# Performance work log

Measured on AMD Instinct MI355X. Metric: run time of the kernel, lower is better.

The kernel has to match this reference:

```python
import math
import jax, jax.numpy as jnp
import numpy as np

N, E = 20000, 640000
S_DIM, Z_DIM, H, QK, VD = 64, 64, 4, 8, 8
EPS = 1e-8


def quat_rotate(v, q):
    # v: [..., 3], q: [..., 4] (w, x, y, z), broadcastable. Unit-quaternion rotation:
    # v' = v + 2*(w*(u x v) + u x (u x v))
    w = q[..., 0:1]
    u = q[..., 1:4]
    uv = jnp.cross(u, v)
    return v + 2.0 * (w * uv + jnp.cross(u, uv))


def setup_inputs() -> dict:
    key = jax.random.key(0)
    ks = jax.random.split(key, 16)
    s = jax.random.normal(ks[0], (N, S_DIM), dtype=jnp.float32)
    z = jax.random.normal(ks[1], (E, Z_DIM), dtype=jnp.float32)
    edge_index = jax.random.randint(ks[2], (2, E), 0, N)
    quaternion = jax.random.normal(ks[3], (N, 4), dtype=jnp.float32)
    quaternion = quaternion / jnp.linalg.norm(quaternion, axis=-1, keepdims=True)
    translation = jax.random.normal(ks[4], (N, 3), dtype=jnp.float32)
    sc_s = 1.0 / math.sqrt(S_DIM)
    sc_z = 1.0 / math.sqrt(Z_DIM)
    # weights stored [in, out] so y = x @ W (equivalent to torch x @ W.T)
    Wq_s = jax.random.normal(ks[5], (S_DIM, H * S_DIM), dtype=jnp.float32) * sc_s
    Wk_s = jax.random.normal(ks[6], (S_DIM, H * S_DIM), dtype=jnp.float32) * sc_s
    Wv_s = jax.random.normal(ks[7], (S_DIM, H * S_DIM), dtype=jnp.float32) * sc_s
    Wq_v = jax.random.normal(ks[8], (S_DIM, H * QK * 3), dtype=jnp.float32) * sc_s
    Wk_v = jax.random.normal(ks[9], (S_DIM, H * QK * 3), dtype=jnp.float32) * sc_s
    Wv_v = jax.random.normal(ks[10], (S_DIM, H * VD * 3), dtype=jnp.float32) * sc_s
    Wb = jax.random.normal(ks[11], (Z_DIM, H), dtype=jnp.float32) * sc_z
    bb = jnp.zeros((H,), dtype=jnp.float32)
    Wdz = jax.random.normal(ks[12], (Z_DIM, Z_DIM // 4), dtype=jnp.float32) * sc_z
    bdz = jnp.zeros((Z_DIM // 4,), dtype=jnp.float32)
    head_weights = jnp.full((H,), 0.541324854612918, dtype=jnp.float32)  # softplus^{-1}(1)
    concat_dim = Z_DIM // 4 + S_DIM + VD * 4
    Wout = jax.random.normal(ks[13], (H * concat_dim, S_DIM), dtype=jnp.float32) / math.sqrt(H * concat_dim)
    bout = jnp.zeros((S_DIM,), dtype=jnp.float32)
    return {
        's': s, 'z': z, 'edge_index': edge_index, 'quaternion': quaternion,
        'translation': translation, 'Wq_s': Wq_s, 'Wk_s': Wk_s, 'Wv_s': Wv_s,
        'Wq_v': Wq_v, 'Wk_v': Wk_v, 'Wv_v': Wv_v, 'Wb': Wb, 'bb': bb,
        'Wdz': Wdz, 'bdz': bdz, 'head_weights': head_weights,
        'Wout': Wout, 'bout': bout,
    }


def reference(s, z, edge_index, quaternion, translation,
              Wq_s, Wk_s, Wv_s, Wq_v, Wk_v, Wv_v,
              Wb, bb, Wdz, bdz, head_weights, Wout, bout):
    idx_i, idx_j = edge_index[0], edge_index[1]
    n = s.shape[0]
    h = head_weights.shape[0]
    qk = Wq_v.shape[1] // (3 * h)
    vd = Wv_v.shape[1] // (3 * h)

    q_scalar = (s @ Wq_s).reshape(n, h, -1)
    k_scalar = (s @ Wk_s).reshape(n, h, -1)
    v_scalar = (s @ Wv_s).reshape(n, h, -1)

    def to_points(x):
        # torch.split into 3 chunks then stack(dim=-1): [n, 3*c] -> [n, c, 3]
        c = x.shape[-1] // 3
        return jnp.swapaxes(x.reshape(n, 3, c), 1, 2)

    quat_b = quaternion[:, None, :]
    trans_b = translation[:, None, :]
    q_vec = (quat_rotate(to_points(s @ Wq_v), quat_b) + trans_b).reshape(n, h, qk, 3)
    k_vec = (quat_rotate(to_points(s @ Wk_v), quat_b) + trans_b).reshape(n, h, qk, 3)
    v_vec = (quat_rotate(to_points(s @ Wv_v), quat_b) + trans_b).reshape(n, h, vd, 3)

    b_bias = z @ Wb + bb  # [E, H]

    attn = jnp.sum(k_scalar[idx_i] * q_scalar[idx_j], axis=-1)  # [E, H]
    attn = attn * math.sqrt(1.0 / 3 * qk) + math.sqrt(1.0 / 3) * b_bias

    disp = q_vec[idx_i] - k_vec[idx_j]            # [E, H, qk, 3]
    vec_att = jnp.sum(disp * disp, axis=-1)       # [E, H, qk]
    hw = jax.nn.softplus(head_weights)[None, :, None]
    vec_att = jnp.sum(vec_att * hw, axis=-1) * math.sqrt(1.0 / (3 * (qk * 9.0 / 2))) * (-0.5)
    attn = attn + vec_att

    # segment softmax over destination node idx_i
    seg_max = jax.ops.segment_max(attn, idx_i, num_segments=n)
    ea = jnp.exp(attn - seg_max[idx_i])
    denom = jax.ops.segment_sum(ea, idx_i, num_segments=n)
    attn = ea / denom[idx_i]                      # [E, H]

    out_scalar = jax.ops.segment_sum(attn[:, :, None] * v_scalar[idx_i], idx_i, num_segments=n)
    out_scalar = out_scalar.reshape(n, -1)

    out_vec = jax.ops.segment_sum(attn[:, :, None, None] * v_vec[idx_i], idx_i, num_segments=n)
    out_vec = out_vec - translation[:, None, None, :]
    q_conj = jnp.concatenate([quaternion[:, :1], -quaternion[:, 1:]], axis=-1)
    out_vec = quat_rotate(out_vec, q_conj[:, None, None, :])   # [n, h, vd, 3]
    out_vec_norm = jnp.sqrt(jnp.sum(out_vec * out_vec, axis=-1) + EPS).reshape(n, -1)
    out_vec_flat = out_vec.reshape(n, -1, 3)

    pair_z = z @ Wdz + bdz                         # [E, z/4]
    out_pair = jax.ops.segment_sum(attn[:, :, None] * pair_z[:, None, :], idx_i, num_segments=n)
    out_pair = out_pair.reshape(n, -1)

    feats = jnp.concatenate([out_scalar,
                             out_vec_flat[..., 0], out_vec_flat[..., 1], out_vec_flat[..., 2],
                             out_vec_norm, out_pair], axis=-1)
    return feats @ Wout + bout
```

## Files before the change

### kernel.cpp

```cpp
#include <hip/hip_runtime.h>
#include <stdint.h>


#define C_SQRT83  1.6329931618554518f
#define C_SQRT13  0.5773502691896258f
#define C_VEC    -0.04811252243246881f

__device__ __forceinline__ unsigned short f2bf(float f){
  unsigned u = __float_as_uint(f);
  u += 0x7fffu + ((u >> 16) & 1u);
  return (unsigned short)(u >> 16);
}
__device__ __forceinline__ unsigned pack2(float a, float b){
  return (unsigned)f2bf(a) | ((unsigned)f2bf(b) << 16);
}
__device__ __forceinline__ float bflo(unsigned u){ return __uint_as_float(u << 16); }
__device__ __forceinline__ float bfhi(unsigned u){ return __uint_as_float(u & 0xffff0000u); }

__device__ __forceinline__ void quat_rot(float w, float ux, float uy, float uz,
                                         float vx, float vy, float vz,
                                         float& ox, float& oy, float& oz){
  float cx = uy*vz - uz*vy;
  float cy = uz*vx - ux*vz;
  float cz = ux*vy - uy*vx;
  float dx = uy*cz - uz*cy;
  float dy = uz*cx - ux*cz;
  float dz = ux*cy - uy*cx;
  ox = vx + 2.f*(w*cx + dx);
  oy = vy + 2.f*(w*cy + dy);
  oz = vz + 2.f*(w*cz + dz);
}


__global__ __launch_bounds__(256) void k_count(const int* __restrict__ ei,
                                               unsigned* __restrict__ counts,
                                               unsigned* __restrict__ rank, int ne){
  int e = blockIdx.x*256 + threadIdx.x;
  if (e >= ne) return;
  rank[e] = atomicAdd(&counts[ei[e]], 1u);
}

__global__ __launch_bounds__(256) void k_scan(const unsigned* __restrict__ counts,
                                              unsigned* __restrict__ row_off, int n){
  __shared__ unsigned part[256];
  int t = threadIdx.x;
  int chunk = (n + 255) >> 8;
  int s0 = t*chunk, s1 = min(s0 + chunk, n);
  unsigned sum = 0;
  for (int k = s0; k < s1; ++k) sum += counts[k];
  part[t] = sum; __syncthreads();
  for (int off = 1; off < 256; off <<= 1){
    unsigned v = (t >= off) ? part[t-off] : 0u;
    __syncthreads();
    part[t] += v;
    __syncthreads();
  }
  unsigned run = (t == 0) ? 0u : part[t-1];
  for (int k = s0; k < s1; ++k){
    row_off[k] = run; run += counts[k];
  }
  if (t == 255) row_off[n] = part[255];
}


#define BN 32

__device__ __forceinline__ void pass256(const float* __restrict__ W,
                                        const float stT[64][40], int cg, int sl,
                                        float acc[8][4]){
  #pragma unroll
  for (int i=0;i<8;i++){ acc[i][0]=0.f; acc[i][1]=0.f; acc[i][2]=0.f; acc[i][3]=0.f; }
  #pragma unroll 4
  for (int k = 0; k < 64; ++k){
    const float4 w  = *(const float4*)(W + (size_t)k*256 + cg*4);
    const float4 n0 = *(const float4*)&stT[k][sl*8];
    const float4 n1 = *(const float4*)&stT[k][sl*8+4];
    acc[0][0]+=n0.x*w.x; acc[0][1]+=n0.x*w.y; acc[0][2]+=n0.x*w.z; acc[0][3]+=n0.x*w.w;
    acc[1][0]+=n0.y*w.x; acc[1][1]+=n0.y*w.y; acc[1][2]+=n0.y*w.z; acc[1][3]+=n0.y*w.w;
    acc[2][0]+=n0.z*w.x; acc[2][1]+=n0.z*w.y; acc[2][2]+=n0.z*w.z; acc[2][3]+=n0.z*w.w;
    acc[3][0]+=n0.w*w.x; acc[3][1]+=n0.w*w.y; acc[3][2]+=n0.w*w.z; acc[3][3]+=n0.w*w.w;
    acc[4][0]+=n1.x*w.x; acc[4][1]+=n1.x*w.y; acc[4][2]+=n1.x*w.z; acc[4][3]+=n1.x*w.w;
    acc[5][0]+=n1.y*w.x; acc[5][1]+=n1.y*w.y; acc[5][2]+=n1.y*w.z; acc[5][3]+=n1.y*w.w;
    acc[6][0]+=n1.z*w.x; acc[6][1]+=n1.z*w.y; acc[6][2]+=n1.z*w.z; acc[6][3]+=n1.z*w.w;
    acc[7][0]+=n1.w*w.x; acc[7][1]+=n1.w*w.y; acc[7][2]+=n1.w*w.z; acc[7][3]+=n1.w*w.w;
  }
}

__device__ __forceinline__ void pass96(const float* __restrict__ W,
                                       const float stT[64][40], int cgp, int slp,
                                       float acc[4][4]){
  #pragma unroll
  for (int i=0;i<4;i++){ acc[i][0]=0.f; acc[i][1]=0.f; acc[i][2]=0.f; acc[i][3]=0.f; }
  if (cgp >= 24) return;
  #pragma unroll 4
  for (int k = 0; k < 64; ++k){
    const float4 w = *(const float4*)(W + (size_t)k*96 + cgp*4);
    const float4 nv = *(const float4*)&stT[k][slp*4];
    acc[0][0]+=nv.x*w.x; acc[0][1]+=nv.x*w.y; acc[0][2]+=nv.x*w.z; acc[0][3]+=nv.x*w.w;
    acc[1][0]+=nv.y*w.x; acc[1][1]+=nv.y*w.y; acc[1][2]+=nv.y*w.z; acc[1][3]+=nv.y*w.w;
    acc[2][0]+=nv.z*w.x; acc[2][1]+=nv.z*w.y; acc[2][2]+=nv.z*w.z; acc[2][3]+=nv.z*w.w;
    acc[3][0]+=nv.w*w.x; acc[3][1]+=nv.w*w.y; acc[3][2]+=nv.w*w.z; acc[3][3]+=nv.w*w.w;
  }
}

__global__ __launch_bounds__(256) void k_proj(
    const float* __restrict__ s, const float* __restrict__ quat, const float* __restrict__ trans,
    const float* __restrict__ Wqs, const float* __restrict__ Wks, const float* __restrict__ Wvs,
    const float* __restrict__ Wqv, const float* __restrict__ Wkv, const float* __restrict__ Wvv,
    unsigned* __restrict__ qs, unsigned* __restrict__ ks, float* __restrict__ vs,
    unsigned* __restrict__ qv, unsigned* __restrict__ kv, float* __restrict__ vv, int n)
{
  __shared__ float stT[64][40];
  __shared__ float pt[BN][97];
  const int tid = threadIdx.x;
  const int node0 = blockIdx.x * BN;

  #pragma unroll
  for (int r = 0; r < 2; ++r){
    const int idx = tid + r*256;
    const int nd = idx >> 4, c4 = idx & 15;
    const int g = node0 + nd;
    float4 v = make_float4(0.f,0.f,0.f,0.f);
    if (g < n) v = *(const float4*)(s + (size_t)g*64 + c4*4);
    stT[c4*4+0][nd]=v.x; stT[c4*4+1][nd]=v.y; stT[c4*4+2][nd]=v.z; stT[c4*4+3][nd]=v.w;
  }
  __syncthreads();

  const int cg = tid & 63, sl = tid >> 6;
  const int cgp = tid & 31, slp = tid >> 5;
  float acc[8][4];

  pass256(Wqs, stT, cg, sl, acc);
  #pragma unroll
  for (int i=0;i<8;i++){
    const int g = node0 + sl*8 + i;
    if (g < n){
      uint2 u; u.x = pack2(acc[i][0],acc[i][1]); u.y = pack2(acc[i][2],acc[i][3]);
      *(uint2*)(qs + (size_t)g*128 + cg*2) = u;
    }
  }
  pass256(Wks, stT, cg, sl, acc);
  #pragma unroll
  for (int i=0;i<8;i++){
    const int g = node0 + sl*8 + i;
    if (g < n){
      uint2 u; u.x = pack2(acc[i][0],acc[i][1]); u.y = pack2(acc[i][2],acc[i][3]);
      *(uint2*)(ks + (size_t)g*128 + cg*2) = u;
    }
  }
  pass256(Wvs, stT, cg, sl, acc);
  #pragma unroll
  for (int i=0;i<8;i++){
    const int g = node0 + sl*8 + i;
    if (g < n){
      float4 f; f.x=acc[i][0]; f.y=acc[i][1]; f.z=acc[i][2]; f.w=acc[i][3];
      *(float4*)(vs + (size_t)g*256 + cg*4) = f;
    }
  }

  float pac[4][4];

  pass96(Wqv, stT, cgp, slp, pac);
  __syncthreads();
  if (cgp < 24){
    #pragma unroll
    for (int i=0;i<4;i++){
      #pragma unroll
      for (int c=0;c<4;c++) pt[slp*4+i][cgp*4+c] = pac[i][c];
    }
  }
  __syncthreads();
  #pragma unroll
  for (int r = 0; r < 2; ++r){
    const int t2 = tid + r*256;
    const int nd = t2 >> 4, pp = t2 & 15;
    const int g = node0 + nd;
    if (g < n){
      const float4 q4 = *(const float4*)(quat + (size_t)g*4);
      const float tx = trans[(size_t)g*3], ty = trans[(size_t)g*3+1], tz = trans[(size_t)g*3+2];
      float x0,y0,z0,x1,y1,z1;
      quat_rot(q4.x,q4.y,q4.z,q4.w, pt[nd][2*pp],   pt[nd][32+2*pp],   pt[nd][64+2*pp],   x0,y0,z0);
      quat_rot(q4.x,q4.y,q4.z,q4.w, pt[nd][2*pp+1], pt[nd][32+2*pp+1], pt[nd][64+2*pp+1], x1,y1,z1);
      x0+=tx; y0+=ty; z0+=tz; x1+=tx; y1+=ty; z1+=tz;
      unsigned* d = qv + (size_t)g*48 + pp*3;
      d[0] = pack2(x0,y0); d[1] = pack2(z0,x1); d[2] = pack2(y1,z1);
    }
  }

  pass96(Wkv, stT, cgp, slp, pac);
  __syncthreads();
  if (cgp < 24){
    #pragma unroll
    for (int i=0;i<4;i++){
      #pragma unroll
      for (int c=0;c<4;c++) pt[slp*4+i][cgp*4+c] = pac[i][c];
    }
  }
  __syncthreads();
  #pragma unroll
  for (int r = 0; r < 2; ++r){
    const int t2 = tid + r*256;
    const int nd = t2 >> 4, pp = t2 & 15;
    const int g = node0 + nd;
    if (g < n){
      const float4 q4 = *(const float4*)(quat + (size_t)g*4);
      const float tx = trans[(size_t)g*3], ty = trans[(size_t)g*3+1], tz = trans[(size_t)g*3+2];
      float x0,y0,z0,x1,y1,z1;
      quat_rot(q4.x,q4.y,q4.z,q4.w, pt[nd][2*pp],   pt[nd][32+2*pp],   pt[nd][64+2*pp],   x0,y0,z0);
      quat_rot(q4.x,q4.y,q4.z,q4.w, pt[nd][2*pp+1], pt[nd][32+2*pp+1], pt[nd][64+2*pp+1], x1,y1,z1);
      x0+=tx; y0+=ty; z0+=tz; x1+=tx; y1+=ty; z1+=tz;
      unsigned* d = kv + (size_t)g*48 + pp*3;
      d[0] = pack2(x0,y0); d[1] = pack2(z0,x1); d[2] = pack2(y1,z1);
    }
  }

  pass96(Wvv, stT, cgp, slp, pac);
  __syncthreads();
  if (cgp < 24){
    #pragma unroll
    for (int i=0;i<4;i++){
      #pragma unroll
      for (int c=0;c<4;c++) pt[slp*4+i][cgp*4+c] = pac[i][c];
    }
  }
  __syncthreads();
  #pragma unroll
  for (int r = 0; r < 12; ++r){
    const int idx = tid + r*256;
    const int nd = idx / 96, col = idx - nd*96;
    const int g = node0 + nd;
    if (g < n) vv[(size_t)g*96 + col] = pt[nd][col];
  }
}


__global__ __launch_bounds__(256) void k_zc(
    const int* __restrict__ ei, const unsigned* __restrict__ rank,
    const unsigned* __restrict__ roff, const float* __restrict__ z,
    const float* __restrict__ Wb,  const float* __restrict__ bb,
    const float* __restrict__ Wdz, const float* __restrict__ bdz,
    const float* __restrict__ hwts,
    const unsigned* __restrict__ qs, const unsigned* __restrict__ ks,
    const unsigned* __restrict__ qv, const unsigned* __restrict__ kv,
    unsigned* __restrict__ rec, int ne)
{
  __shared__ float zT[2][16][258];
  const int tid = threadIdx.x;
  const int E0  = blockIdx.x * 256;
  const int e   = E0 + tid;
  const bool full = (E0 + 256 <= ne);

  int i = 0, j = 0; unsigned pos = 0;
  if (e < ne){
    i = ei[e]; j = ei[ne + e];
    pos = roff[i] + rank[e];
  }

  const float hw0 = C_VEC * log1pf(__expf(hwts[0]));
  const float hw1 = C_VEC * log1pf(__expf(hwts[1]));
  const float hw2 = C_VEC * log1pf(__expf(hwts[2]));
  const float hw3 = C_VEC * log1pf(__expf(hwts[3]));

  float b4[4] = {0.f,0.f,0.f,0.f};
  float pacc[16];
  #pragma unroll
  for (int c=0;c<16;c++) pacc[c]=0.f;

  if (full){
    #pragma unroll
    for (int q = 0; q < 4; ++q){
      const int idx = tid + q*256;
      const int row = idx >> 2, f4 = idx & 3;
      const float4 v = *(const float4*)(z + (size_t)(E0+row)*64 + f4*4);
      zT[0][f4*4+0][row]=v.x; zT[0][f4*4+1][row]=v.y;
      zT[0][f4*4+2][row]=v.z; zT[0][f4*4+3][row]=v.w;
    }
    __syncthreads();
    #pragma unroll
    for (int c = 0; c < 4; ++c){
      if (c < 3){
        const int nb = (c+1)&1;
        #pragma unroll
        for (int q = 0; q < 4; ++q){
          const int idx = tid + q*256;
          const int row = idx >> 2, f4 = idx & 3;
          const float4 v = *(const float4*)(z + (size_t)(E0+row)*64 + (c+1)*16 + f4*4);
          zT[nb][f4*4+0][row]=v.x; zT[nb][f4*4+1][row]=v.y;
          zT[nb][f4*4+2][row]=v.z; zT[nb][f4*4+3][row]=v.w;
        }
      }
      const int kb = c*16, buf = c&1;
      #pragma unroll
      for (int kk = 0; kk < 16; ++kk){
        const float zk = zT[buf][kk][tid];
        const int k = kb + kk;
        const float4 wb = *(const float4*)(Wb + k*4);
        b4[0]+=zk*wb.x; b4[1]+=zk*wb.y; b4[2]+=zk*wb.z; b4[3]+=zk*wb.w;
        const float* wd = Wdz + k*16;
        const float4 w0=*(const float4*)(wd),   w1=*(const float4*)(wd+4),
                     w2=*(const float4*)(wd+8), w3=*(const float4*)(wd+12);
        pacc[ 0]+=zk*w0.x; pacc[ 1]+=zk*w0.y; pacc[ 2]+=zk*w0.z; pacc[ 3]+=zk*w0.w;
        pacc[ 4]+=zk*w1.x; pacc[ 5]+=zk*w1.y; pacc[ 6]+=zk*w1.z; pacc[ 7]+=zk*w1.w;
        pacc[ 8]+=zk*w2.x; pacc[ 9]+=zk*w2.y; pacc[10]+=zk*w2.z; pacc[11]+=zk*w2.w;
        pacc[12]+=zk*w3.x; pacc[13]+=zk*w3.y; pacc[14]+=zk*w3.z; pacc[15]+=zk*w3.w;
      }
      __syncthreads();
    }
  } else if (e < ne){
    const float* zr = z + (size_t)e*64;
    for (int k4 = 0; k4 < 16; ++k4){
      const float4 zv = *(const float4*)(zr + 4*k4);
      #pragma unroll
      for (int kk = 0; kk < 4; ++kk){
        const int k = 4*k4 + kk;
        const float zk = (kk==0)?zv.x:((kk==1)?zv.y:((kk==2)?zv.z:zv.w));
        const float4 wb = *(const float4*)(Wb + k*4);
        b4[0]+=zk*wb.x; b4[1]+=zk*wb.y; b4[2]+=zk*wb.z; b4[3]+=zk*wb.w;
        const float* wd = Wdz + k*16;
        const float4 w0=*(const float4*)(wd),   w1=*(const float4*)(wd+4),
                     w2=*(const float4*)(wd+8), w3=*(const float4*)(wd+12);
        pacc[ 0]+=zk*w0.x; pacc[ 1]+=zk*w0.y; pacc[ 2]+=zk*w0.z; pacc[ 3]+=zk*w0.w;
        pacc[ 4]+=zk*w1.x; pacc[ 5]+=zk*w1.y; pacc[ 6]+=zk*w1.z; pacc[ 7]+=zk*w1.w;
        pacc[ 8]+=zk*w2.x; pacc[ 9]+=zk*w2.y; pacc[10]+=zk*w2.z; pacc[11]+=zk*w2.w;
        pacc[12]+=zk*w3.x; pacc[13]+=zk*w3.y; pacc[14]+=zk*w3.z; pacc[15]+=zk*w3.w;
      }
    }
  }

  uint4 u0, u1;
  float bl0=0.f, bl1=0.f, bl2=0.f, bl3=0.f;
  if (e < ne){
    #pragma unroll
    for (int c=0;c<16;c++) pacc[c] += bdz[c];
    u0.x=pack2(pacc[0],pacc[1]);   u0.y=pack2(pacc[2],pacc[3]);
    u0.z=pack2(pacc[4],pacc[5]);   u0.w=pack2(pacc[6],pacc[7]);
    u1.x=pack2(pacc[8],pacc[9]);   u1.y=pack2(pacc[10],pacc[11]);
    u1.z=pack2(pacc[12],pacc[13]); u1.w=pack2(pacc[14],pacc[15]);
    bl0 = C_SQRT13*(b4[0] + bb[0]);
    bl1 = C_SQRT13*(b4[1] + bb[1]);
    bl2 = C_SQRT13*(b4[2] + bb[2]);
    bl3 = C_SQRT13*(b4[3] + bb[3]);
  } else {
    u0 = make_uint4(0,0,0,0); u1 = make_uint4(0,0,0,0);
  }

  if (full){
    const int l = tid & 63;
    const int c = l & 3, g = l >> 2;
    #pragma unroll
    for (int sb = 0; sb < 4; ++sb){
      const int el = sb*16 + g;
      const int ie = __shfl(i, el, 64);
      const int je = __shfl(j, el, 64);

      const uint4* kr = (const uint4*)ks + (size_t)ie*32;
      const uint4* qr = (const uint4*)qs + (size_t)je*32;
      float s0=0.f, s1=0.f, s2=0.f, s3=0.f;
      #pragma unroll
      for (int it = 0; it < 8; ++it){
        const uint4 a = kr[it*4 + c];
        const uint4 b = qr[it*4 + c];
        float d;
        d  = bflo(a.x)*bflo(b.x) + bfhi(a.x)*bfhi(b.x);
        d += bflo(a.y)*bflo(b.y) + bfhi(a.y)*bfhi(b.y);
        d += bflo(a.z)*bflo(b.z) + bfhi(a.z)*bfhi(b.z);
        d += bflo(a.w)*bflo(b.w) + bfhi(a.w)*bfhi(b.w);
        if      (it < 2) s0 += d;
        else if (it < 4) s1 += d;
        else if (it < 6) s2 += d;
        else             s3 += d;
      }

      const uint4* qvr = (const uint4*)qv + (size_t)ie*12;
      const uint4* kvr = (const uint4*)kv + (size_t)je*12;
      float v0=0.f, v1=0.f, v2=0.f, v3=0.f;
      {
        const uint4 a = qvr[c], b = kvr[c];
        float d, t;
        t = bflo(a.x)-bflo(b.x); d  = t*t;  t = bfhi(a.x)-bfhi(b.x); d += t*t;
        t = bflo(a.y)-bflo(b.y); d += t*t;  t = bfhi(a.y)-bfhi(b.y); d += t*t;
        t = bflo(a.z)-bflo(b.z); d += t*t;  t = bfhi(a.z)-bfhi(b.z); d += t*t;
        t = bflo(a.w)-bflo(b.w); d += t*t;  t = bfhi(a.w)-bfhi(b.w); d += t*t;
        if (c < 3) v0 += d; else v1 += d;
      }
      {
        const uint4 a = qvr[4+c], b = kvr[4+c];
        float d, t;
        t = bflo(a.x)-bflo(b.x); d  = t*t;  t = bfhi(a.x)-bfhi(b.x); d += t*t;
        t = bflo(a.y)-bflo(b.y); d += t*t;  t = bfhi(a.y)-bfhi(b.y); d += t*t;
        t = bflo(a.z)-bflo(b.z); d += t*t;  t = bfhi(a.z)-bfhi(b.z); d += t*t;
        t = bflo(a.w)-bflo(b.w); d += t*t;  t = bfhi(a.w)-bfhi(b.w); d += t*t;
        if (c < 2) v1 += d; else v2 += d;
      }
      {
        const uint4 a = qvr[8+c], b = kvr[8+c];
        float d, t;
        t = bflo(a.x)-bflo(b.x); d  = t*t;  t = bfhi(a.x)-bfhi(b.x); d += t*t;
        t = bflo(a.y)-bflo(b.y); d += t*t;  t = bfhi(a.y)-bfhi(b.y); d += t*t;
        t = bflo(a.z)-bflo(b.z); d += t*t;  t = bfhi(a.z)-bfhi(b.z); d += t*t;
        t = bflo(a.w)-bflo(b.w); d += t*t;  t = bfhi(a.w)-bfhi(b.w); d += t*t;
        if (c < 1) v2 += d; else v3 += d;
      }

      float p0 = C_SQRT83*s0 + hw0*v0;
      float p1 = C_SQRT83*s1 + hw1*v1;
      float p2 = C_SQRT83*s2 + hw2*v2;
      float p3 = C_SQRT83*s3 + hw3*v3;
      #pragma unroll
      for (int msk = 1; msk < 4; msk <<= 1){
        p0 += __shfl_xor(p0, msk, 64);
        p1 += __shfl_xor(p1, msk, 64);
        p2 += __shfl_xor(p2, msk, 64);
        p3 += __shfl_xor(p3, msk, 64);
      }
      const float pc = (c==0)?p0:((c==1)?p1:((c==2)?p2:p3));

      const int srcbase = (l & 15) << 2;
      const float q0 = __shfl(pc, srcbase+0, 64);
      const float q1 = __shfl(pc, srcbase+1, 64);
      const float q2 = __shfl(pc, srcbase+2, 64);
      const float q3 = __shfl(pc, srcbase+3, 64);
      if ((l >> 4) == sb){
        uint4* d = (uint4*)rec + (size_t)pos*4;
        float4 lg; lg.x = q0 + bl0; lg.y = q1 + bl1; lg.z = q2 + bl2; lg.w = q3 + bl3;
        d[0] = *(uint4*)&lg;
        d[1] = u0;
        d[2] = u1;
      }
    }
  } else if (e < ne){
    const uint4* kr = (const uint4*)ks + (size_t)i*32;
    const uint4* qr = (const uint4*)qs + (size_t)j*32;
    float sdot[4];
    #pragma unroll
    for (int h = 0; h < 4; ++h){
      float acc = 0.f;
      #pragma unroll
      for (int cc = 0; cc < 8; ++cc){
        const uint4 a = kr[h*8+cc];
        const uint4 b = qr[h*8+cc];
        acc += bflo(a.x)*bflo(b.x) + bfhi(a.x)*bfhi(b.x);
        acc += bflo(a.y)*bflo(b.y) + bfhi(a.y)*bfhi(b.y);
        acc += bflo(a.z)*bflo(b.z) + bfhi(a.z)*bfhi(b.z);
        acc += bflo(a.w)*bflo(b.w) + bfhi(a.w)*bfhi(b.w);
      }
      sdot[h] = acc;
    }
    const uint4* qvr = (const uint4*)qv + (size_t)i*12;
    const uint4* kvr = (const uint4*)kv + (size_t)j*12;
    float vsum[4];
    #pragma unroll
    for (int h = 0; h < 4; ++h){
      float acc = 0.f;
      #pragma unroll
      for (int cc = 0; cc < 3; ++cc){
        const uint4 a = qvr[h*3+cc];
        const uint4 b = kvr[h*3+cc];
        float d;
        d = bflo(a.x)-bflo(b.x); acc += d*d;  d = bfhi(a.x)-bfhi(b.x); acc += d*d;
        d = bflo(a.y)-bflo(b.y); acc += d*d;  d = bfhi(a.y)-bfhi(b.y); acc += d*d;
        d = bflo(a.z)-bflo(b.z); acc += d*d;  d = bfhi(a.z)-bfhi(b.z); acc += d*d;
        d = bflo(a.w)-bflo(b.w); acc += d*d;  d = bfhi(a.w)-bfhi(b.w); acc += d*d;
      }
      vsum[h] = acc;
    }
    float4 lg;
    lg.x = C_SQRT83*sdot[0] + bl0 + hw0*vsum[0];
    lg.y = C_SQRT83*sdot[1] + bl1 + hw1*vsum[1];
    lg.z = C_SQRT83*sdot[2] + bl2 + hw2*vsum[2];
    lg.w = C_SQRT83*sdot[3] + bl3 + hw3*vsum[3];
    uint4* d = (uint4*)rec + (size_t)pos*4;
    d[0] = *(uint4*)&lg;
    d[1] = u0;
    d[2] = u1;
  }
}


__global__ __launch_bounds__(256) void k_soft(
    const unsigned* __restrict__ rec,
    const unsigned* __restrict__ row_off, float* __restrict__ out_pair, int n)
{
  const int node = blockIdx.x*4 + (threadIdx.x >> 6);
  if (node >= n) return;
  const int lane = threadIdx.x & 63;
  const int beg = (int)row_off[node], end = (int)row_off[node+1];
  const float* recf = (const float*)rec;

  float m[4] = {-3.0e38f,-3.0e38f,-3.0e38f,-3.0e38f};
  for (int p = beg + lane; p < end; p += 64){
    const float4 l = *(const float4*)(recf + (size_t)p*16);
    m[0]=fmaxf(m[0],l.x); m[1]=fmaxf(m[1],l.y); m[2]=fmaxf(m[2],l.z); m[3]=fmaxf(m[3],l.w);
  }
  #pragma unroll
  for (int msk = 1; msk < 64; msk <<= 1){
    #pragma unroll
    for (int h=0;h<4;h++) m[h] = fmaxf(m[h], __shfl_xor(m[h], msk));
  }
  float S[4] = {0.f,0.f,0.f,0.f};
  for (int p = beg + lane; p < end; p += 64){
    const float4 l = *(const float4*)(recf + (size_t)p*16);
    S[0]+=__expf(l.x-m[0]); S[1]+=__expf(l.y-m[1]);
    S[2]+=__expf(l.z-m[2]); S[3]+=__expf(l.w-m[3]);
  }
  #pragma unroll
  for (int msk = 1; msk < 64; msk <<= 1){
    #pragma unroll
    for (int h=0;h<4;h++) S[h] += __shfl_xor(S[h], msk);
  }
  float inv[4];
  #pragma unroll
  for (int h=0;h<4;h++) inv[h] = (S[h] > 0.f) ? (1.f/S[h]) : 0.f;

  const int e4 = lane >> 4, c = lane & 15;
  float acc[4] = {0.f,0.f,0.f,0.f};
  for (int base = beg; base < end; base += 4){
    const int p = base + e4;
    if (p < end){
      const float4 l = *(const float4*)(recf + (size_t)p*16);
      const unsigned u = rec[(size_t)p*16 + 4 + (c>>1)];
      const float pzv = (c & 1) ? bfhi(u) : bflo(u);
      acc[0] += __expf(l.x-m[0]) * pzv;
      acc[1] += __expf(l.y-m[1]) * pzv;
      acc[2] += __expf(l.z-m[2]) * pzv;
      acc[3] += __expf(l.w-m[3]) * pzv;
    }
  }
  #pragma unroll
  for (int msk = 16; msk < 64; msk <<= 1){
    #pragma unroll
    for (int h=0;h<4;h++) acc[h] += __shfl_xor(acc[h], msk);
  }
  const int hOut = lane >> 4;
  out_pair[(size_t)node*64 + lane] = acc[hOut] * inv[hOut];
}


__global__ __launch_bounds__(256) void k_out(
    const float* __restrict__ vs, const float* __restrict__ vv,
    const float* __restrict__ out_pair, const unsigned* __restrict__ row_off,
    const float* __restrict__ quat, const float* __restrict__ trans,
    const float* __restrict__ Wout, const float* __restrict__ bout,
    float* __restrict__ out, int n)
{
  __shared__ float feats[32][448];
  __shared__ int degs[32];
  const int tid = threadIdx.x;
  const int node0 = blockIdx.x*32;

  if (tid < 32){
    const int g = node0 + tid;
    degs[tid] = (g < n) ? (int)(row_off[g+1] - row_off[g]) : 1;
  }
  __syncthreads();

  for (int x = tid; x < 32*256; x += 256){
    const int nd = x >> 8, c = x & 255;
    const int g = node0 + nd;
    feats[nd][c] = (g < n && degs[nd] > 0) ? vs[(size_t)g*256 + c] : 0.f;
  }
  for (int x = tid; x < 32*64; x += 256){
    const int nd = x >> 6, c = x & 63;
    const int g = node0 + nd;
    feats[nd][384 + c] = (g < n) ? out_pair[(size_t)g*64 + c] : 0.f;
  }
  for (int x = tid; x < 32*32; x += 256){
    const int nd = x >> 5, pt = x & 31;
    const int g = node0 + nd;
    float X=0.f, Y=0.f, Z=0.f;
    if (g < n){
      if (degs[nd] > 0){
        X = vv[(size_t)g*96 + pt];
        Y = vv[(size_t)g*96 + 32 + pt];
        Z = vv[(size_t)g*96 + 64 + pt];
      } else {
        const float4 q4 = *(const float4*)(quat + (size_t)g*4);
        const float tx = trans[(size_t)g*3], ty = trans[(size_t)g*3+1], tz = trans[(size_t)g*3+2];
        quat_rot(q4.x, -q4.y, -q4.z, -q4.w, -tx, -ty, -tz, X, Y, Z);
      }
    }
    feats[nd][256 + pt] = X;
    feats[nd][288 + pt] = Y;
    feats[nd][320 + pt] = Z;
    feats[nd][352 + pt] = sqrtf(X*X + Y*Y + Z*Z + 1e-8f);
  }
  __syncthreads();

  const int lane = tid & 63;
  const int wave = tid >> 6;
  float acc[8];
  #pragma unroll
  for (int q8=0;q8<8;q8++) acc[q8]=0.f;

  for (int k0 = 0; k0 < 448; k0 += 4){
    const float w0 = Wout[(size_t)(k0+0)*64 + lane];
    const float w1 = Wout[(size_t)(k0+1)*64 + lane];
    const float w2 = Wout[(size_t)(k0+2)*64 + lane];
    const float w3 = Wout[(size_t)(k0+3)*64 + lane];
    #pragma unroll
    for (int q8 = 0; q8 < 8; ++q8){
      const float4 f = *(const float4*)&feats[wave*8 + q8][k0];
      acc[q8] += f.x*w0 + f.y*w1 + f.z*w2 + f.w*w3;
    }
  }
  const float bo = bout[lane];
  #pragma unroll
  for (int q8 = 0; q8 < 8; ++q8){
    const int g = node0 + wave*8 + q8;
    if (g < n) out[(size_t)g*64 + lane] = acc[q8] + bo;
  }
}


extern "C" void kernel_launch(void* const* d_in, const int* in_sizes, int n_in,
                              void* d_out, int out_size, void* d_ws, size_t ws_size,
                              hipStream_t stream) {
  const float* s     = (const float*)d_in[0];
  const float* z     = (const float*)d_in[1];
  const int*   ei    = (const int*)  d_in[2];
  const float* quat  = (const float*)d_in[3];
  const float* trans = (const float*)d_in[4];
  const float* Wqs   = (const float*)d_in[5];
  const float* Wks   = (const float*)d_in[6];
  const float* Wvs   = (const float*)d_in[7];
  const float* Wqv   = (const float*)d_in[8];
  const float* Wkv   = (const float*)d_in[9];
  const float* Wvv   = (const float*)d_in[10];
  const float* Wb    = (const float*)d_in[11];
  const float* bb    = (const float*)d_in[12];
  const float* Wdz   = (const float*)d_in[13];
  const float* bdz   = (const float*)d_in[14];
  const float* hwts  = (const float*)d_in[15];
  const float* Wout  = (const float*)d_in[16];
  const float* bout  = (const float*)d_in[17];
  float* out = (float*)d_out;

  const int n  = in_sizes[0] / 64;
  const int ne = in_sizes[1] / 64;

  size_t off = 0;
  char* base = (char*)d_ws;
  auto take = [&](size_t bytes)->char* {
    char* p = base + off;
    off += (bytes + 255) & ~(size_t)255;
    return p;
  };
  unsigned* qs     = (unsigned*)take((size_t)n*512);
  unsigned* ks     = (unsigned*)take((size_t)n*512);
  unsigned* qvt    = (unsigned*)take((size_t)n*192);
  unsigned* kvt    = (unsigned*)take((size_t)n*192);
  float*    vs     = (float*)   take((size_t)n*1024);
  float*    vv     = (float*)   take((size_t)n*384);
  unsigned* rec    = (unsigned*)take((size_t)ne*64);
  unsigned* counts = (unsigned*)take((size_t)n*4);
  unsigned* roff   = (unsigned*)take((size_t)(n+1)*4);
  unsigned* rank   = (unsigned*)take((size_t)ne*4);
  float*    opair  = (float*)   take((size_t)n*256);
  (void)ws_size; (void)n_in; (void)out_size;

  const int gbE = (ne + 255) / 256;

  hipMemsetAsync(counts, 0, (size_t)n*4, stream);
  k_count<<<gbE, 256, 0, stream>>>(ei, counts, rank, ne);
  k_scan <<<1,   256, 0, stream>>>(counts, roff, n);
  k_proj <<<(n + BN - 1)/BN, 256, 0, stream>>>(s, quat, trans, Wqs, Wks, Wvs, Wqv, Wkv, Wvv,
                                               qs, ks, vs, qvt, kvt, vv, n);
  k_zc   <<<gbE, 256, 0, stream>>>(ei, rank, roff, z, Wb, bb, Wdz, bdz, hwts,
                                   qs, ks, qvt, kvt, rec, ne);
  k_soft <<<(n + 3)/4, 256, 0, stream>>>(rec, roff, opair, n);
  k_out  <<<(n + 31)/32, 256, 0, stream>>>(vs, vv, opair, roff, quat, trans,
                                           Wout, bout, out, n);
}
```

Before: 617.0 us.

## Split edge kernel into z-feature pass and sorted-order attention logit pass

Result: faster. 598.3 us (-3.0%).

```diff
diff --git a/kernel.cpp b/kernel.cpp
--- a/kernel.cpp
+++ b/kernel.cpp
@@ -234,17 +234,14 @@
 }
 
 
-__global__ __launch_bounds__(256) void k_zc(
+__global__ __launch_bounds__(256) void k_zf(
     const int* __restrict__ ei, const unsigned* __restrict__ rank,
     const unsigned* __restrict__ roff, const float* __restrict__ z,
     const float* __restrict__ Wb,  const float* __restrict__ bb,
     const float* __restrict__ Wdz, const float* __restrict__ bdz,
-    const float* __restrict__ hwts,
-    const unsigned* __restrict__ qs, const unsigned* __restrict__ ks,
-    const unsigned* __restrict__ qv, const unsigned* __restrict__ kv,
     unsigned* __restrict__ rec, int ne)
 {
-  __shared__ float zT[2][16][258];
+  __shared__ float zT[16][258];
   const int tid = threadIdx.x;
   const int E0  = blockIdx.x * 256;
   const int e   = E0 + tid;
@@ -256,11 +253,6 @@
     pos = roff[i] + rank[e];
   }
 
-  const float hw0 = C_VEC * log1pf(__expf(hwts[0]));
-  const float hw1 = C_VEC * log1pf(__expf(hwts[1]));
-  const float hw2 = C_VEC * log1pf(__expf(hwts[2]));
-  const float hw3 = C_VEC * log1pf(__expf(hwts[3]));
-
   float b4[4] = {0.f,0.f,0.f,0.f};
   float pacc[16];
   #pragma unroll
@@ -268,31 +260,21 @@
 
   if (full){
     #pragma unroll
-    for (int q = 0; q < 4; ++q){
-      const int idx = tid + q*256;
-      const int row = idx >> 2, f4 = idx & 3;
-      const float4 v = *(const float4*)(z + (size_t)(E0+row)*64 + f4*4);
-      zT[0][f4*4+0][row]=v.x; zT[0][f4*4+1][row]=v.y;
-      zT[0][f4*4+2][row]=v.z; zT[0][f4*4+3][row]=v.w;
-    }
-    __syncthreads();
-    #pragma unroll
     for (int c = 0; c < 4; ++c){
-      if (c < 3){
-        const int nb = (c+1)&1;
-        #pragma unroll
-        for (int q = 0; q < 4; ++q){
-          const int idx = tid + q*256;
-          const int row = idx >> 2, f4 = idx & 3;
-          const float4 v = *(const float4*)(z + (size_t)(E0+row)*64 + (c+1)*16 + f4*4);
-          zT[nb][f4*4+0][row]=v.x; zT[nb][f4*4+1][row]=v.y;
-          zT[nb][f4*4+2][row]=v.z; zT[nb][f4*4+3][row]=v.w;
-        }
-      }
-      const int kb = c*16, buf = c&1;
+      if (c) __syncthreads();
+      #pragma unroll
+      for (int q = 0; q < 4; ++q){
+        const int idx = tid + q*256;
+        const int row = idx >> 2, f4 = idx & 3;
+        const float4 v = *(const float4*)(z + (size_t)(E0+row)*64 + c*16 + f4*4);
+        zT[f4*4+0][row]=v.x; zT[f4*4+1][row]=v.y;
+        zT[f4*4+2][row]=v.z; zT[f4*4+3][row]=v.w;
+      }
+      __syncthreads();
+      const int kb = c*16;
       #pragma unroll
       for (int kk = 0; kk < 16; ++kk){
-        const float zk = zT[buf][kk][tid];
+        const float zk = zT[kk][tid];
         const int k = kb + kk;
         const float4 wb = *(const float4*)(Wb + k*4);
         b4[0]+=zk*wb.x; b4[1]+=zk*wb.y; b4[2]+=zk*wb.z; b4[3]+=zk*wb.w;
@@ -304,7 +286,6 @@
         pacc[ 8]+=zk*w2.x; pacc[ 9]+=zk*w2.y; pacc[10]+=zk*w2.z; pacc[11]+=zk*w2.w;
         pacc[12]+=zk*w3.x; pacc[13]+=zk*w3.y; pacc[14]+=zk*w3.z; pacc[15]+=zk*w3.w;
       }
-      __syncthreads();
     }
   } else if (e < ne){
     const float* zr = z + (size_t)e*64;
@@ -327,21 +308,50 @@
     }
   }
 
-  uint4 u0, u1;
-  float bl0=0.f, bl1=0.f, bl2=0.f, bl3=0.f;
   if (e < ne){
     #pragma unroll
     for (int c=0;c<16;c++) pacc[c] += bdz[c];
+    uint4 u0, u1;
     u0.x=pack2(pacc[0],pacc[1]);   u0.y=pack2(pacc[2],pacc[3]);
     u0.z=pack2(pacc[4],pacc[5]);   u0.w=pack2(pacc[6],pacc[7]);
     u1.x=pack2(pacc[8],pacc[9]);   u1.y=pack2(pacc[10],pacc[11]);
     u1.z=pack2(pacc[12],pacc[13]); u1.w=pack2(pacc[14],pacc[15]);
-    bl0 = C_SQRT13*(b4[0] + bb[0]);
-    bl1 = C_SQRT13*(b4[1] + bb[1]);
-    bl2 = C_SQRT13*(b4[2] + bb[2]);
-    bl3 = C_SQRT13*(b4[3] + bb[3]);
-  } else {
-    u0 = make_uint4(0,0,0,0); u1 = make_uint4(0,0,0,0);
+    float4 bo;
+    bo.x = C_SQRT13*(b4[0] + bb[0]);
+    bo.y = C_SQRT13*(b4[1] + bb[1]);
+    bo.z = C_SQRT13*(b4[2] + bb[2]);
+    bo.w = C_SQRT13*(b4[3] + bb[3]);
+    uint4* d = (uint4*)rec + (size_t)pos*4;
+    d[0] = *(uint4*)&bo;
+    d[1] = u0;
+    d[2] = u1;
+    d[3] = make_uint4((unsigned)i, (unsigned)j, 0u, 0u);
+  }
+}
+
+
+__global__ __launch_bounds__(256) void k_edge(
+    const float* __restrict__ hwts,
+    const unsigned* __restrict__ qs, const unsigned* __restrict__ ks,
+    const unsigned* __restrict__ qv, const unsigned* __restrict__ kv,
+    unsigned* __restrict__ rec, int ne)
+{
+  const int tid = threadIdx.x;
+  const int P0  = blockIdx.x * 256;
+  const int p   = P0 + tid;
+  const bool full = (P0 + 256 <= ne);
+
+  const float hw0 = C_VEC * log1pf(__expf(hwts[0]));
+  const float hw1 = C_VEC * log1pf(__expf(hwts[1]));
+  const float hw2 = C_VEC * log1pf(__expf(hwts[2]));
+  const float hw3 = C_VEC * log1pf(__expf(hwts[3]));
+
+  int i = 0, j = 0;
+  float4 bias = make_float4(0.f,0.f,0.f,0.f);
+  if (p < ne){
+    bias = *(const float4*)((const float*)rec + (size_t)p*16);
+    const uint2 ij = *(const uint2*)(rec + (size_t)p*16 + 12);
+    i = (int)ij.x; j = (int)ij.y;
   }
 
   if (full){
@@ -421,14 +431,12 @@
       const float q2 = __shfl(pc, srcbase+2, 64);
       const float q3 = __shfl(pc, srcbase+3, 64);
       if ((l >> 4) == sb){
-        uint4* d = (uint4*)rec + (size_t)pos*4;
-        float4 lg; lg.x = q0 + bl0; lg.y = q1 + bl1; lg.z = q2 + bl2; lg.w = q3 + bl3;
-        d[0] = *(uint4*)&lg;
-        d[1] = u0;
-        d[2] = u1;
-      }
-    }
-  } else if (e < ne){
+        float4 lg; lg.x = q0 + bias.x; lg.y = q1 + bias.y;
+        lg.z = q2 + bias.z; lg.w = q3 + bias.w;
+        *((uint4*)rec + (size_t)p*4) = *(uint4*)&lg;
+      }
+    }
+  } else if (p < ne){
     const uint4* kr = (const uint4*)ks + (size_t)i*32;
     const uint4* qr = (const uint4*)qs + (size_t)j*32;
     float sdot[4];
@@ -465,14 +473,11 @@
       vsum[h] = acc;
     }
     float4 lg;
-    lg.x = C_SQRT83*sdot[0] + bl0 + hw0*vsum[0];
-    lg.y = C_SQRT83*sdot[1] + bl1 + hw1*vsum[1];
-    lg.z = C_SQRT83*sdot[2] + bl2 + hw2*vsum[2];
-    lg.w = C_SQRT83*sdot[3] + bl3 + hw3*vsum[3];
-    uint4* d = (uint4*)rec + (size_t)pos*4;
-    d[0] = *(uint4*)&lg;
-    d[1] = u0;
-    d[2] = u1;
+    lg.x = C_SQRT83*sdot[0] + bias.x + hw0*vsum[0];
+    lg.y = C_SQRT83*sdot[1] + bias.y + hw1*vsum[1];
+    lg.z = C_SQRT83*sdot[2] + bias.z + hw2*vsum[2];
+    lg.w = C_SQRT83*sdot[3] + bias.w + hw3*vsum[3];
+    *((uint4*)rec + (size_t)p*4) = *(uint4*)&lg;
   }
 }
 
@@ -665,8 +670,8 @@
   k_scan <<<1,   256, 0, stream>>>(counts, roff, n);
   k_proj <<<(n + BN - 1)/BN, 256, 0, stream>>>(s, quat, trans, Wqs, Wks, Wvs, Wqv, Wkv, Wvv,
                                                qs, ks, vs, qvt, kvt, vv, n);
-  k_zc   <<<gbE, 256, 0, stream>>>(ei, rank, roff, z, Wb, bb, Wdz, bdz, hwts,
-                                   qs, ks, qvt, kvt, rec, ne);
+  k_zf   <<<gbE, 256, 0, stream>>>(ei, rank, roff, z, Wb, bb, Wdz, bdz, rec, ne);
+  k_edge <<<gbE, 256, 0, stream>>>(hwts, qs, ks, qvt, kvt, rec, ne);
   k_soft <<<(n + 3)/4, 256, 0, stream>>>(rec, roff, opair, n);
   k_out  <<<(n + 31)/32, 256, 0, stream>>>(vs, vv, opair, roff, quat, trans,
                                            Wout, bout, out, n);
```
